# Kernel optimization log

Measured on AMD Instinct MI355X. Metric: run time of the kernel, lower is better.

The kernel has to match this reference:

```python
import jax, jax.numpy as jnp
import numpy as np
from jax import lax

H = 64  # hidden_dim


def lstm_layer(xs, W_ih, W_hh, b_ih, b_hh):
    """PyTorch-convention LSTM layer. xs: [B,T,I]. Gate order i,f,g,o."""
    B = xs.shape[0]
    # Precompute input contribution for all timesteps: [B,T,4H]
    xg = jnp.einsum('bti,gi->btg', xs, W_ih) + b_ih + b_hh
    h0 = jnp.zeros((B, H), xs.dtype)
    c0 = jnp.zeros((B, H), xs.dtype)

    def step(carry, xg_t):
        h, c = carry
        gates = xg_t + h @ W_hh.T  # [B,4H]
        i, f, g, o = jnp.split(gates, 4, axis=-1)
        i = jax.nn.sigmoid(i)
        f = jax.nn.sigmoid(f)
        g = jnp.tanh(g)
        o = jax.nn.sigmoid(o)
        c = f * c + i * g
        h = o * jnp.tanh(c)
        return (h, c), h

    (_, _), hs = lax.scan(step, (h0, c0), jnp.swapaxes(xg, 0, 1))  # hs: [T,B,H]
    return jnp.swapaxes(hs, 0, 1)  # [B,T,H]


def setup_inputs() -> dict:
    key = jax.random.key(0)
    ks = jax.random.split(key, 12)
    B, T = 2048, 512
    s = 1.0 / np.sqrt(H)  # PyTorch default init scale
    u = lambda k, shape: jax.random.uniform(k, shape, jnp.float32, -s, s)
    return {
        'x': jax.random.normal(ks[0], (B, T), jnp.float32),
        'W_ih0': u(ks[1], (4 * H, 1)),
        'W_hh0': u(ks[2], (4 * H, H)),
        'b_ih0': u(ks[3], (4 * H,)),
        'b_hh0': u(ks[4], (4 * H,)),
        'W_ih1': u(ks[5], (4 * H, H)),
        'W_hh1': u(ks[6], (4 * H, H)),
        'b_ih1': u(ks[7], (4 * H,)),
        'b_hh1': u(ks[8], (4 * H,)),
        'fc_W': u(ks[9], (1, H)),
        'fc_b': u(ks[10], (1,)),
    }


def reference(x, W_ih0, W_hh0, b_ih0, b_hh0, W_ih1, W_hh1, b_ih1, b_hh1, fc_W, fc_b):
    xs = x[..., None]  # [B,T,1]
    h1 = lstm_layer(xs, W_ih0, W_hh0, b_ih0, b_hh0)   # [B,T,H]
    h2 = lstm_layer(h1, W_ih1, W_hh1, b_ih1, b_hh1)   # [B,T,H]
    out = h2[:, -1, :] @ fc_W.T + fc_b                 # [B,1]
    return out[:, 0]                                   # [B]
```

## Files before the change

kernel.cpp:

```cpp
#include <hip/hip_runtime.h>

namespace {

constexpr int TT = 512;
constexpr int H  = 64;
constexpr int NB = 8;
constexpr int NT = 512;
constexpr float L2E = 1.442695041f;

typedef float  f32x4  __attribute__((ext_vector_type(4)));
typedef short  bf16x8 __attribute__((ext_vector_type(8)));

#define MFMA(A, B, C) (C) = __builtin_amdgcn_mfma_f32_16x16x32_bf16((A), (B), (C), 0, 0, 0)

__device__ __forceinline__ float exp2_hw(float x) {
    float r; asm("v_exp_f32 %0, %1" : "=v"(r) : "v"(x)); return r;
}
__device__ __forceinline__ float sigm_pre(float zs) {
    return __builtin_amdgcn_rcpf(1.0f + exp2_hw(zs));
}
__device__ __forceinline__ float tanh_pre(float zs) {
    return fmaf(2.0f, __builtin_amdgcn_rcpf(1.0f + exp2_hw(zs)), -1.0f);
}
__device__ __forceinline__ float tanh_fast(float z) {
    return fmaf(2.0f, __builtin_amdgcn_rcpf(1.0f + exp2_hw(-2.885390082f * z)), -1.0f);
}
__device__ __forceinline__ unsigned short f2bf(float f) {
    unsigned u = __float_as_uint(f);
    return (unsigned short)((u + 0x7fffu + ((u >> 16) & 1u)) >> 16);
}
__device__ __forceinline__ float bf2f(unsigned short s) {
    return __uint_as_float(((unsigned)s) << 16);
}

__device__ __forceinline__ void waitge(int* c, int v) {
    while (__hip_atomic_load(c, __ATOMIC_ACQUIRE, __HIP_MEMORY_SCOPE_WORKGROUP) < v) {}
}
__device__ __forceinline__ void signal(int* c) {
    if ((threadIdx.x & 63) == 0)
        (void)__hip_atomic_fetch_add(c, 1, __ATOMIC_RELEASE, __HIP_MEMORY_SCOPE_WORKGROUP);
}


__global__ void prep_weights(const float* __restrict__ W_hh0,
                             const float* __restrict__ W_ih1,
                             const float* __restrict__ W_hh1,
                             unsigned short* __restrict__ ws)
{
    const int id = blockIdx.x * blockDim.x + threadIdx.x;
    int wl, lane, i, j, kt;
    const float* src;
    size_t dst;
    if (id < 2048) {
        wl = id >> 9; lane = (id >> 3) & 63; i = id & 7;
        j = i >> 1; kt = i & 1;
        const int lr = lane & 15, lg = lane >> 4;
        const int row = j * 64 + 16 * wl + lr;
        src = W_hh0 + row * 64 + kt * 32 + lg * 8;
        dst = (size_t)((wl * 64 + lane) * 8 + i) * 16;
    } else {
        const int id2 = id - 2048;
        wl = id2 >> 10; lane = (id2 >> 4) & 63; i = id2 & 15;
        j = i >> 2; kt = i & 3;
        const int lr = lane & 15, lg = lane >> 4;
        const int row = j * 64 + 16 * wl + lr;
        src = (kt < 2) ? (W_ih1 + row * 64 + kt * 32 + lg * 8)
                       : (W_hh1 + row * 64 + (kt - 2) * 32 + lg * 8);
        dst = 32768 + (size_t)((wl * 64 + lane) * 16 + i) * 16;
    }
    const float sj = (j == 2) ? (-2.0f * L2E) : (-L2E);
    float4 a = *(const float4*)src;
    float4 b = *(const float4*)(src + 4);
    float t[8] = {a.x * sj, a.y * sj, a.z * sj, a.w * sj,
                  b.x * sj, b.y * sj, b.z * sj, b.w * sj};
    bf16x8 hi, lo;
    #pragma unroll
    for (int e = 0; e < 8; ++e) {
        unsigned short h = f2bf(t[e]);
        hi[e] = (short)h;
        lo[e] = (short)f2bf(t[e] - bf2f(h));
    }
    *(bf16x8*)(ws + dst)     = hi;
    *(bf16x8*)(ws + dst + 8) = lo;
}

__global__ __launch_bounds__(NT)
__attribute__((amdgpu_waves_per_eu(2, 2)))
void lstm2_mfma_kernel(
    const float* __restrict__ x,
    const unsigned short* __restrict__ wfrag,
    const float* __restrict__ W_ih0,
    const float* __restrict__ b_ih0, const float* __restrict__ b_hh0,
    const float* __restrict__ b_ih1, const float* __restrict__ b_hh1,
    const float* __restrict__ fc_W,  const float* __restrict__ fc_b,
    float* __restrict__ out)
{
    __shared__ alignas(16) unsigned short h1ring[4][1024];
    __shared__ alignas(16) unsigned short h2buf[2][1024];
    __shared__ float x_lds2[TT][NB];
    __shared__ float fc_part[32][NB];
    __shared__ int c0, c1c, c1d;

    const int tid  = threadIdx.x;
    const int lane = tid & 63;
    const int wid  = tid >> 6;
    const int wloc = wid & 3;
    const bool isL1 = wid >= 4;
    const int lr = lane & 15;
    const int lg = lane >> 4;
    const int b0 = blockIdx.x * NB;
    const bool lo8 = (lr < 8);
    const int rb = lo8 ? 0 : 2;

    {
        const float4* xs = (const float4*)(x + (size_t)b0 * TT);
        #pragma unroll
        for (int i = 0; i < 2; ++i) {
            int idx = i * NT + tid;
            float4 v = xs[idx];
            int b  = idx >> 7;
            int t4 = (idx & 127) << 2;
            x_lds2[t4 + 0][b] = v.x;
            x_lds2[t4 + 1][b] = v.y;
            x_lds2[t4 + 2][b] = v.z;
            x_lds2[t4 + 3][b] = v.w;
        }
    }
    {
        int* hz = (int*)h1ring;
        #pragma unroll
        for (int i = 0; i < 4; ++i) hz[i * NT + tid] = 0;
        int* h2z = (int*)h2buf;
        #pragma unroll
        for (int i = 0; i < 2; ++i) h2z[i * NT + tid] = 0;
    }
    if (tid == 0) { c0 = 0; c1c = 0; c1d = 0; }

    bf16x8 Ahi[16];
    float bias[16], wxv[16];
    float cst0 = 0.f, cst1 = 0.f;
    const int base_u = 16 * wloc + 4 * lg;
    const int u0 = base_u + rb;
    const int wo  = ((lr & 7) + 16 * (base_u >> 3)) * 8 + (base_u & 7) + rb;
    const int fro = lane * 8;

    if (!isL1) {
        const unsigned short* wb = wfrag + ((wloc * 64 + lane) << 7);
        #pragma unroll
        for (int i = 0; i < 8; ++i)
            Ahi[i] = *(const bf16x8*)(wb + i * 16);
        #pragma unroll
        for (int j = 0; j < 4; ++j) {
            const float sj = (j == 2) ? (-2.0f * L2E) : (-L2E);
            const int rowc = j * 64 + base_u;
            #pragma unroll
            for (int r = 0; r < 4; ++r) {
                bias[j * 4 + r] = (b_ih0[rowc + r] + b_hh0[rowc + r]) * sj;
                wxv [j * 4 + r] = W_ih0[rowc + r] * sj;
            }
        }
    } else {
        const unsigned short* wb = wfrag + 32768 + ((wloc * 64 + lane) << 8);
        #pragma unroll
        for (int i = 0; i < 16; ++i)
            Ahi[i] = *(const bf16x8*)(wb + i * 16);
        #pragma unroll
        for (int j = 0; j < 4; ++j) {
            const float sj = (j == 2) ? (-2.0f * L2E) : (-L2E);
            const int rowc = j * 64 + base_u;
            #pragma unroll
            for (int r = 0; r < 4; ++r)
                bias[j * 4 + r] = (b_ih1[rowc + r] + b_hh1[rowc + r]) * sj;
        }
    }

    __syncthreads();

    if (!isL1) {
        for (int t = 0; t < TT; ++t) {
            const float xv = x_lds2[t][lane & 7];
            f32x4 acc[4];
            #pragma unroll
            for (int j = 0; j < 4; ++j)
                #pragma unroll
                for (int r = 0; r < 4; ++r)
                    acc[j][r] = fmaf(wxv[j * 4 + r], xv, bias[j * 4 + r]);
            if (t >= 4) waitge(&c1c, 4 * (t - 3));
            waitge(&c0, 4 * t);
            const unsigned short* ph = &h1ring[(t - 1) & 3][0];
            bf16x8 Bh0 = *(const bf16x8*)(ph + fro);
            bf16x8 Bh1 = *(const bf16x8*)(ph + 512 + fro);
            #pragma unroll
            for (int j = 0; j < 4; ++j) MFMA(Ahi[j * 2 + 0], Bh0, acc[j]);
            #pragma unroll
            for (int j = 0; j < 4; ++j) MFMA(Ahi[j * 2 + 1], Bh1, acc[j]);
            const float zi0 = lo8 ? acc[0][0] : acc[0][2];
            const float zi1 = lo8 ? acc[0][1] : acc[0][3];
            const float zf0 = lo8 ? acc[1][0] : acc[1][2];
            const float zf1 = lo8 ? acc[1][1] : acc[1][3];
            const float zg0 = lo8 ? acc[2][0] : acc[2][2];
            const float zg1 = lo8 ? acc[2][1] : acc[2][3];
            const float zo0 = lo8 ? acc[3][0] : acc[3][2];
            const float zo1 = lo8 ? acc[3][1] : acc[3][3];
            cst0 = fmaf(sigm_pre(zf0), cst0, sigm_pre(zi0) * tanh_pre(zg0));
            cst1 = fmaf(sigm_pre(zf1), cst1, sigm_pre(zi1) * tanh_pre(zg1));
            const float hv0 = sigm_pre(zo0) * tanh_fast(cst0);
            const float hv1 = sigm_pre(zo1) * tanh_fast(cst1);
            unsigned p;
            asm("v_cvt_pk_bf16_f32 %0, %1, %2" : "=v"(p) : "v"(hv0), "v"(hv1));
            *(unsigned*)&h1ring[t & 3][wo]      = p;
            *(unsigned*)&h1ring[t & 3][wo + 64] = p;
            signal(&c0);
        }
    } else {
        f32x4 acc[4];
        bf16x8 B0, B1;
        waitge(&c0, 4);
        {
            const unsigned short* p1 = &h1ring[0][0];
            B0 = *(const bf16x8*)(p1 + fro);
            B1 = *(const bf16x8*)(p1 + 512 + fro);
        }
        signal(&c1c);
        #pragma unroll
        for (int j = 0; j < 4; ++j)
            #pragma unroll
            for (int r = 0; r < 4; ++r)
                acc[j][r] = bias[j * 4 + r];
        #pragma unroll
        for (int j = 0; j < 4; ++j) MFMA(Ahi[j * 4 + 0], B0, acc[j]);
        #pragma unroll
        for (int j = 0; j < 4; ++j) MFMA(Ahi[j * 4 + 1], B1, acc[j]);

        for (int t = 1; t <= TT; ++t) {
            waitge(&c1d, 4 * (t - 1));
            const unsigned short* p2 = &h2buf[(t - 2) & 1][0];
            bf16x8 B2 = *(const bf16x8*)(p2 + fro);
            bf16x8 B3 = *(const bf16x8*)(p2 + 512 + fro);
            #pragma unroll
            for (int j = 0; j < 4; ++j) MFMA(Ahi[j * 4 + 2], B2, acc[j]);
            #pragma unroll
            for (int j = 0; j < 4; ++j) MFMA(Ahi[j * 4 + 3], B3, acc[j]);
            const float zi0 = lo8 ? acc[0][0] : acc[0][2];
            const float zi1 = lo8 ? acc[0][1] : acc[0][3];
            const float zf0 = lo8 ? acc[1][0] : acc[1][2];
            const float zf1 = lo8 ? acc[1][1] : acc[1][3];
            const float zg0 = lo8 ? acc[2][0] : acc[2][2];
            const float zg1 = lo8 ? acc[2][1] : acc[2][3];
            const float zo0 = lo8 ? acc[3][0] : acc[3][2];
            const float zo1 = lo8 ? acc[3][1] : acc[3][3];
            cst0 = fmaf(sigm_pre(zf0), cst0, sigm_pre(zi0) * tanh_pre(zg0));
            cst1 = fmaf(sigm_pre(zf1), cst1, sigm_pre(zi1) * tanh_pre(zg1));
            const float hv0 = sigm_pre(zo0) * tanh_fast(cst0);
            const float hv1 = sigm_pre(zo1) * tanh_fast(cst1);
            unsigned p;
            asm("v_cvt_pk_bf16_f32 %0, %1, %2" : "=v"(p) : "v"(hv0), "v"(hv1));
            *(unsigned*)&h2buf[(t - 1) & 1][wo]      = p;
            *(unsigned*)&h2buf[(t - 1) & 1][wo + 64] = p;
            signal(&c1d);
            if (t < TT) {
                waitge(&c0, 4 * (t + 1));
                const unsigned short* p1 = &h1ring[t & 3][0];
                B0 = *(const bf16x8*)(p1 + fro);
                B1 = *(const bf16x8*)(p1 + 512 + fro);
                signal(&c1c);
                #pragma unroll
                for (int j = 0; j < 4; ++j)
                    #pragma unroll
                    for (int r = 0; r < 4; ++r)
                        acc[j][r] = bias[j * 4 + r];
                #pragma unroll
                for (int j = 0; j < 4; ++j) MFMA(Ahi[j * 4 + 0], B0, acc[j]);
                #pragma unroll
                for (int j = 0; j < 4; ++j) MFMA(Ahi[j * 4 + 1], B1, acc[j]);
            } else {
                const float s = fc_W[u0] * hv0 + fc_W[u0 + 1] * hv1;
                fc_part[(wid - 4) * 8 + lg * 2 + (lo8 ? 0 : 1)][lr & 7] = s;
            }
        }
    }

    __syncthreads();

    if (tid < NB) {
        float s = fc_b[0];
        #pragma unroll
        for (int i = 0; i < 32; ++i) s += fc_part[i][tid];
        out[b0 + tid] = s;
    }
}

}

extern "C" void kernel_launch(void* const* d_in, const int* in_sizes, int n_in,
                              void* d_out, int out_size, void* d_ws, size_t ws_size,
                              hipStream_t stream)
{
    const float* x     = (const float*)d_in[0];
    const float* W_ih0 = (const float*)d_in[1];
    const float* W_hh0 = (const float*)d_in[2];
    const float* b_ih0 = (const float*)d_in[3];
    const float* b_hh0 = (const float*)d_in[4];
    const float* W_ih1 = (const float*)d_in[5];
    const float* W_hh1 = (const float*)d_in[6];
    const float* b_ih1 = (const float*)d_in[7];
    const float* b_hh1 = (const float*)d_in[8];
    const float* fc_W  = (const float*)d_in[9];
    const float* fc_b  = (const float*)d_in[10];
    float* out = (float*)d_out;
    unsigned short* ws = (unsigned short*)d_ws;

    hipLaunchKernelGGL(prep_weights, dim3(24), dim3(256), 0, stream,
                       W_hh0, W_ih1, W_hh1, ws);

    const int B = in_sizes[0] / TT;
    dim3 grid(B / NB), block(NT);
    hipLaunchKernelGGL(lstm2_mfma_kernel, grid, block, 0, stream,
                       x, ws, W_ih0, b_ih0, b_hh0, b_ih1, b_hh1, fc_W, fc_b, out);
}
```

Before: 336.7 us.

## Merge LSTM gate reciprocals, drop duplicate h stores, feed bias directly into MFMA

The gate activations are rewritten so that sigmoid(i)*tanh(g) and sigmoid(o)*tanh(c) each need one reciprocal of a product instead of two separate reciprocals. This trims transcendental work on the serial recurrence path. Each h value is now stored once instead of twice, and lanes 8-15 read the same LDS fragment address through a masked offset. Layer 1 also passes a bias vector straight in as the MFMA accumulator input instead of copying it element by element. The risks are overflow to inf in products of exponentials for large pre-activations, and LDS bank conflicts from the changed read pattern.

```diff
diff --git a/kernel.cpp b/kernel.cpp
--- a/kernel.cpp
+++ b/kernel.cpp
@@ -16,14 +16,17 @@
 __device__ __forceinline__ float exp2_hw(float x) {
     float r; asm("v_exp_f32 %0, %1" : "=v"(r) : "v"(x)); return r;
 }
-__device__ __forceinline__ float sigm_pre(float zs) {
-    return __builtin_amdgcn_rcpf(1.0f + exp2_hw(zs));
-}
-__device__ __forceinline__ float tanh_pre(float zs) {
-    return fmaf(2.0f, __builtin_amdgcn_rcpf(1.0f + exp2_hw(zs)), -1.0f);
-}
-__device__ __forceinline__ float tanh_fast(float z) {
-    return fmaf(2.0f, __builtin_amdgcn_rcpf(1.0f + exp2_hw(-2.885390082f * z)), -1.0f);
+__device__ __forceinline__ float act_pair(float zi, float zf, float zg, float zo,
+                                          float& c) {
+    const float ei = exp2_hw(zi);
+    const float ef = exp2_hw(zf);
+    const float eg = exp2_hw(zg);
+    const float eo = exp2_hw(zo);
+    const float sf = __builtin_amdgcn_rcpf(1.0f + ef);
+    const float P  = (1.0f - eg) * __builtin_amdgcn_rcpf((1.0f + ei) * (1.0f + eg));
+    c = fmaf(sf, c, P);
+    const float ec = exp2_hw(-2.885390082f * c);
+    return (1.0f - ec) * __builtin_amdgcn_rcpf((1.0f + eo) * (1.0f + ec));
 }
 __device__ __forceinline__ unsigned short f2bf(float f) {
     unsigned u = __float_as_uint(f);
@@ -138,11 +141,12 @@
 
     bf16x8 Ahi[16];
     float bias[16], wxv[16];
+    f32x4 bias4[4];
     float cst0 = 0.f, cst1 = 0.f;
     const int base_u = 16 * wloc + 4 * lg;
     const int u0 = base_u + rb;
     const int wo  = ((lr & 7) + 16 * (base_u >> 3)) * 8 + (base_u & 7) + rb;
-    const int fro = lane * 8;
+    const int fro = (lane & ~8) * 8;
 
     if (!isL1) {
         const unsigned short* wb = wfrag + ((wloc * 64 + lane) << 7);
@@ -170,7 +174,7 @@
             const int rowc = j * 64 + base_u;
             #pragma unroll
             for (int r = 0; r < 4; ++r)
-                bias[j * 4 + r] = (b_ih1[rowc + r] + b_hh1[rowc + r]) * sj;
+                bias4[j][r] = (b_ih1[rowc + r] + b_hh1[rowc + r]) * sj;
         }
     }
 
@@ -202,14 +206,11 @@
             const float zg1 = lo8 ? acc[2][1] : acc[2][3];
             const float zo0 = lo8 ? acc[3][0] : acc[3][2];
             const float zo1 = lo8 ? acc[3][1] : acc[3][3];
-            cst0 = fmaf(sigm_pre(zf0), cst0, sigm_pre(zi0) * tanh_pre(zg0));
-            cst1 = fmaf(sigm_pre(zf1), cst1, sigm_pre(zi1) * tanh_pre(zg1));
-            const float hv0 = sigm_pre(zo0) * tanh_fast(cst0);
-            const float hv1 = sigm_pre(zo1) * tanh_fast(cst1);
+            const float hv0 = act_pair(zi0, zf0, zg0, zo0, cst0);
+            const float hv1 = act_pair(zi1, zf1, zg1, zo1, cst1);
             unsigned p;
             asm("v_cvt_pk_bf16_f32 %0, %1, %2" : "=v"(p) : "v"(hv0), "v"(hv1));
-            *(unsigned*)&h1ring[t & 3][wo]      = p;
-            *(unsigned*)&h1ring[t & 3][wo + 64] = p;
+            *(unsigned*)&h1ring[t & 3][wo] = p;
             signal(&c0);
         }
     } else {
@@ -224,11 +225,8 @@
         signal(&c1c);
         #pragma unroll
         for (int j = 0; j < 4; ++j)
-            #pragma unroll
-            for (int r = 0; r < 4; ++r)
-                acc[j][r] = bias[j * 4 + r];
-        #pragma unroll
-        for (int j = 0; j < 4; ++j) MFMA(Ahi[j * 4 + 0], B0, acc[j]);
+            acc[j] = __builtin_amdgcn_mfma_f32_16x16x32_bf16(Ahi[j * 4 + 0], B0,
+                                                             bias4[j], 0, 0, 0);
         #pragma unroll
         for (int j = 0; j < 4; ++j) MFMA(Ahi[j * 4 + 1], B1, acc[j]);
 
@@ -249,14 +247,11 @@
             const float zg1 = lo8 ? acc[2][1] : acc[2][3];
             const float zo0 = lo8 ? acc[3][0] : acc[3][2];
             const float zo1 = lo8 ? acc[3][1] : acc[3][3];
-            cst0 = fmaf(sigm_pre(zf0), cst0, sigm_pre(zi0) * tanh_pre(zg0));
-            cst1 = fmaf(sigm_pre(zf1), cst1, sigm_pre(zi1) * tanh_pre(zg1));
-            const float hv0 = sigm_pre(zo0) * tanh_fast(cst0);
-            const float hv1 = sigm_pre(zo1) * tanh_fast(cst1);
+            const float hv0 = act_pair(zi0, zf0, zg0, zo0, cst0);
+            const float hv1 = act_pair(zi1, zf1, zg1, zo1, cst1);
             unsigned p;
             asm("v_cvt_pk_bf16_f32 %0, %1, %2" : "=v"(p) : "v"(hv0), "v"(hv1));
-            *(unsigned*)&h2buf[(t - 1) & 1][wo]      = p;
-            *(unsigned*)&h2buf[(t - 1) & 1][wo + 64] = p;
+            *(unsigned*)&h2buf[(t - 1) & 1][wo] = p;
             signal(&c1d);
             if (t < TT) {
                 waitge(&c0, 4 * (t + 1));
@@ -266,11 +261,9 @@
                 signal(&c1c);
                 #pragma unroll
                 for (int j = 0; j < 4; ++j)
-                    #pragma unroll
-                    for (int r = 0; r < 4; ++r)
-                        acc[j][r] = bias[j * 4 + r];
-                #pragma unroll
-                for (int j = 0; j < 4; ++j) MFMA(Ahi[j * 4 + 0], B0, acc[j]);
+                    acc[j] = __builtin_amdgcn_mfma_f32_16x16x32_bf16(Ahi[j * 4 + 0],
+                                                                     B0, bias4[j],
+                                                                     0, 0, 0);
                 #pragma unroll
                 for (int j = 0; j < 4; ++j) MFMA(Ahi[j * 4 + 1], B1, acc[j]);
             } else {
```

Measured after the change: 329.9 us (median of 2 runs). 1.02x faster.
